# Kernel optimization log

Measured on AMD Instinct MI355X. Metric: run time of the kernel, lower is better.

The kernel has to match this reference:

```python
import jax, jax.numpy as jnp
import numpy as np

H = 64          # hidden_dim
NH = 4          # n_heads
DH = H // NH
F_OWN = 40      # own feature dim
FA = 24         # ally feature dim
FE = 24         # enemy feature dim
NAL = 15        # n_allies
NEN = 16        # n_enemies
BS = 2048       # episode batch
NAG = 16        # n_agents
BN = BS * NAG
AMOVE = 6       # normal (move) actions
HYPER_OUT = F_OWN * H + H + 4


def setup_inputs():
    key = jax.random.key(0)
    ks = jax.random.split(key, 32)
    g = lambda k, sh, s=1.0: jax.random.normal(k, sh, dtype=jnp.float32) * s
    inv = lambda d: float(1.0 / np.sqrt(d))
    return {
        "own_raw": g(ks[0], (BN, 1, F_OWN)),
        "ally_raw": g(ks[1], (BN, NAL, FA)),
        "enemy_raw": g(ks[2], (BN, NEN, FE)),
        "hidden_state": g(ks[3], (BN, H)),
        "hyp_W1": g(ks[4], (F_OWN, H), inv(F_OWN)),
        "hyp_b1": jnp.zeros((H,), jnp.float32),
        "hyp_W2": g(ks[5], (H, HYPER_OUT), 0.01 * inv(H)),  # torch init mul_(0.01)
        "hyp_b2": jnp.zeros((HYPER_OUT,), jnp.float32),
        "Wa": g(ks[6], (FA, H), inv(FA)), "ba": jnp.zeros((H,), jnp.float32),
        "We": g(ks[7], (FE, H), inv(FE)), "be": jnp.zeros((H,), jnp.float32),
        "aWq": g(ks[8], (H, H), inv(H)), "aWk": g(ks[9], (H, H), inv(H)),
        "aWv": g(ks[10], (H, H), inv(H)), "aWo": g(ks[11], (H, H), inv(H)),
        "eWq": g(ks[12], (H, H), inv(H)), "eWk": g(ks[13], (H, H), inv(H)),
        "eWv": g(ks[14], (H, H), inv(H)), "eWo": g(ks[15], (H, H), inv(H)),
        "gru_Wih": g(ks[16], (3 * H, 3 * H), inv(3 * H)),
        "gru_Whh": g(ks[17], (H, 3 * H), inv(H)),
        "gru_bih": jnp.zeros((3 * H,), jnp.float32),
        "gru_bhh": jnp.zeros((3 * H,), jnp.float32),
        "Wm": g(ks[18], (H, AMOVE), inv(H)), "bm": jnp.zeros((AMOVE,), jnp.float32),
        "WzK": g(ks[19], (H, H), inv(H)),
        "WEK": g(ks[20], (H, H), inv(H)),
        "bs": BS,
    }


def _mha(q_in, kv, mask, Wq, Wk, Wv, Wo):
    # masked multi-head cross attention: q_in [B,H], kv [B,n,H], mask [B,n] bool
    B, n = kv.shape[0], kv.shape[1]
    q = (q_in @ Wq).reshape(B, NH, DH)
    k = (kv @ Wk).reshape(B, n, NH, DH)
    v = (kv @ Wv).reshape(B, n, NH, DH)
    scores = jnp.einsum('bhd,bnhd->bhn', q, k) * float(1.0 / np.sqrt(DH))
    scores = jnp.where(mask[:, None, :], scores, -1e9)
    attn = jax.nn.softmax(scores, axis=-1)
    out = jnp.einsum('bhn,bnhd->bhd', attn, v).reshape(B, H)
    return out @ Wo


def reference(own_raw, ally_raw, enemy_raw, hidden_state,
              hyp_W1, hyp_b1, hyp_W2, hyp_b2,
              Wa, ba, We, be,
              aWq, aWk, aWv, aWo, eWq, eWk, eWv, eWo,
              gru_Wih, gru_Whh, gru_bih, gru_bhh,
              Wm, bm, WzK, WEK, bs):
    Bn = own_raw.shape[0]
    ally_mask = jnp.any(ally_raw != 0, axis=-1)    # ~all(x==0)
    enemy_mask = jnp.any(enemy_raw != 0, axis=-1)
    own_vec = own_raw[:, 0, :]                     # [Bn, F_OWN]
    # hypernet: per-agent own-embedding weights + bias (last 4 outputs unused, as in source)
    h_out = jax.nn.relu(own_vec @ hyp_W1 + hyp_b1) @ hyp_W2 + hyp_b2
    W_flat = h_out[:, :F_OWN * H].reshape(Bn, F_OWN, H)
    b_own = h_out[:, F_OWN * H:F_OWN * H + H]
    own_e = jnp.einsum('bf,bfh->bh', own_vec, W_flat) + b_own
    ally_e = ally_raw @ Wa + ba
    enemy_e = enemy_raw @ We + be
    zA = _mha(own_e, ally_e, ally_mask, aWq, aWk, aWv, aWo)
    zE = _mha(own_e, enemy_e, enemy_mask, eWq, eWk, eWv, eWo)
    u_cat = jnp.concatenate([own_e, zA, zE], axis=-1)  # [Bn, 3H]
    # GRUCell (torch semantics)
    gx = u_cat @ gru_Wih + gru_bih
    gh = hidden_state @ gru_Whh + gru_bhh
    xr, xz, xn = jnp.split(gx, 3, axis=-1)
    hr, hz, hn = jnp.split(gh, 3, axis=-1)
    r = jax.nn.sigmoid(xr + hr)
    zg = jax.nn.sigmoid(xz + hz)
    ncand = jnp.tanh(xn + r * hn)
    z = (1.0 - zg) * ncand + zg * hidden_state
    logits_move = z @ Wm + bm
    zk = z @ WzK
    Ek = enemy_e @ WEK
    logits_shoot = jnp.einsum('bd,bmd->bm', zk, Ek)
    Q = jnp.concatenate([logits_move, logits_shoot], axis=-1)[:, None, :]
    return Q, z.reshape(bs, -1, H)
```

## Files before the change

### kernel.cpp

```cpp
#include <hip/hip_runtime.h>
#include <hip/hip_bf16.h>
#include <math.h>

#define TB 32
#define LOG2E 1.44269504f

typedef float f32x4 __attribute__((ext_vector_type(4)));
typedef _Float16 f16x8 __attribute__((ext_vector_type(8)));
typedef _Float16 f16x4 __attribute__((ext_vector_type(4)));
typedef _Float16 f16x2 __attribute__((ext_vector_type(2)));

#define OFF_W1T  344064
#define OFF_WOA  352256
#define OFF_WOE  360448
#define OFF_VBA  368640
#define OFF_VBE  372736
#define OFF_GA   376832
#define OFF_GE   393216
#define OFF_GIH  409600
#define OFF_GHH  483328
#define OFF_GBS  507904
#define OFF_GBH  508672
#define OFF_BHD  508928

#define MFH(a, b, c) __builtin_amdgcn_mfma_f32_16x16x32_f16((a), (b), (c), 0, 0, 0)

__device__ inline float dot2(f16x2 a, f16x2 b, float c) {
#if __has_builtin(__builtin_amdgcn_fdot2)
  return __builtin_amdgcn_fdot2(a, b, c, false);
#else
  return c + (float)a[0] * (float)b[0] + (float)a[1] * (float)b[1];
#endif
}
__device__ inline f16x2 pk2(float x, float y) {
  f16x2 r; r[0] = (_Float16)x; r[1] = (_Float16)y; return r;
}

__global__ __launch_bounds__(256)
void prep_kernel(const float* __restrict__ hyp_W1, const float* __restrict__ hyp_b1,
                 const float* __restrict__ hyp_W2, const float* __restrict__ hyp_b2,
                 const float* __restrict__ Wa, const float* __restrict__ ba,
                 const float* __restrict__ We, const float* __restrict__ be,
                 const float* __restrict__ aWq, const float* __restrict__ aWk,
                 const float* __restrict__ aWv, const float* __restrict__ aWo,
                 const float* __restrict__ eWq, const float* __restrict__ eWk,
                 const float* __restrict__ eWv, const float* __restrict__ eWo,
                 const float* __restrict__ gWih, const float* __restrict__ gWhh,
                 const float* __restrict__ gbih, const float* __restrict__ gbhh,
                 const float* __restrict__ WzK, const float* __restrict__ WEK,
                 const float* __restrict__ Wm,
                 void* __restrict__ ws)
{
  const int b = blockIdx.x, t = threadIdx.x;
  if (b < 42) {
    _Float16* o = (_Float16*)ws;
    for (int i = t; i < 4096; i += 256) {
      int h = i >> 6, k = i & 63;
      float v;
      if (b < 40)       v = hyp_W2[(size_t)k * 2628 + b * 64 + h];
      else if (b == 40) v = hyp_W2[(size_t)k * 2628 + 2560 + h];
      else              v = (k < 40) ? hyp_b2[k * 64 + h]
                             : (k == 40 ? hyp_b2[2560 + h] : 0.0f);
      o[b * 4096 + i] = (_Float16)v;
    }
  } else if (b == 42) {
    _Float16* o = (_Float16*)((char*)ws + OFF_W1T);
    for (int i = t; i < 4096; i += 256) {
      int h = i >> 6, k = i & 63;
      float v = (k < 40) ? hyp_W1[k * 64 + h] : (k == 40 ? hyp_b1[h] : 0.0f);
      o[i] = (_Float16)v;
    }
  } else if (b == 43 || b == 44) {
    const float* M = (b == 43) ? aWo : eWo;
    _Float16* o = (_Float16*)((char*)ws + (b == 43 ? OFF_WOA : OFF_WOE));
    for (int i = t; i < 4096; i += 256)
      o[i] = (_Float16)M[(i & 63) * 64 + (i >> 6)];
  } else if (b == 45 || b == 46) {
    const float* Wemb = (b == 45) ? Wa : We;
    const float* bemb = (b == 45) ? ba : be;
    const float* Wv   = (b == 45) ? aWv : eWv;
    _Float16* o = (_Float16*)((char*)ws + (b == 45 ? OFF_VBA : OFF_VBE));
    for (int i = t; i < 2048; i += 256) {
      int h = i >> 5, k = i & 31;
      float v = 0.f;
      if (k < 24)       { for (int d = 0; d < 64; ++d) v += Wemb[k * 64 + d] * Wv[d * 64 + h]; }
      else if (k == 24) { for (int d = 0; d < 64; ++d) v += bemb[d] * Wv[d * 64 + h]; }
      o[i] = (_Float16)v;
    }
  } else if (b == 47 || b == 48) {
    const float* Wemb = (b == 47) ? Wa : We;
    const float* bemb = (b == 47) ? ba : be;
    const float* Wk   = (b == 47) ? aWk : eWk;
    const float* Wq   = (b == 47) ? aWq : eWq;
    _Float16* o = (_Float16*)((char*)ws + (b == 47 ? OFF_GA : OFF_GE));
    __shared__ float sKb[25 * 64];
    for (int i = t; i < 1600; i += 256) {
      int k = i >> 6, c = i & 63;
      float v = 0.f;
      if (k < 24)  { for (int d = 0; d < 64; ++d) v += Wemb[k * 64 + d] * Wk[d * 64 + c]; }
      else         { for (int d = 0; d < 64; ++d) v += bemb[d] * Wk[d * 64 + c]; }
      sKb[i] = v;
    }
    __syncthreads();
    for (int i = t; i < 8192; i += 256) {
      int col = i >> 6, d = i & 63;
      int h = col >> 5, kk = col & 31;
      float v = 0.f;
      if (kk < 25)
        for (int dh = 0; dh < 16; ++dh)
          v += Wq[d * 64 + h * 16 + dh] * sKb[kk * 64 + h * 16 + dh];
      o[i] = (_Float16)(v * 0.25f * LOG2E);
    }
  } else if (b == 49) {
    _Float16* o = (_Float16*)((char*)ws + OFF_GIH);
    for (int i = t; i < 36864; i += 256) {
      int d = i / 192, c = i - d * 192;
      o[c * 192 + d] = (_Float16)gWih[i];
    }
  } else if (b == 50) {
    _Float16* o = (_Float16*)((char*)ws + OFF_GHH);
    for (int i = t; i < 12288; i += 256) {
      int d = i / 192, c = i - d * 192;
      o[c * 64 + d] = (_Float16)gWhh[i];
    }
  } else if (b == 51) {
    float* gbS = (float*)((char*)ws + OFF_GBS);
    float* gbH = (float*)((char*)ws + OFF_GBH);
    if (t < 192) gbS[t] = gbih[t] + (t < 128 ? gbhh[t] : 0.0f);
    if (t < 64)  gbH[t] = gbhh[128 + t];
  } else if (b == 52) {
    __shared__ float sWsK[24 * 64];
    __shared__ float sbw[64];
    _Float16* o = (_Float16*)((char*)ws + OFF_BHD);
    for (int i = t; i < 1536; i += 256) {
      int j = i >> 6, h = i & 63;
      float v = 0.f;
      for (int c = 0; c < 64; ++c) v += We[j * 64 + c] * WEK[c * 64 + h];
      sWsK[i] = v;
    }
    if (t < 64) {
      float v = 0.f;
      for (int c = 0; c < 64; ++c) v += be[c] * WEK[c * 64 + t];
      sbw[t] = v;
    }
    __syncthreads();
    for (int i = t; i < 2048; i += 256) {
      int col = i >> 6, c = i & 63;
      float v = 0.f;
      if (col < 24)       { for (int d = 0; d < 64; ++d) v += WzK[c * 64 + d] * sWsK[col * 64 + d]; }
      else if (col == 24) { for (int d = 0; d < 64; ++d) v += WzK[c * 64 + d] * sbw[d]; }
      else if (col < 31)  v = Wm[c * 6 + (col - 25)];
      o[i] = (_Float16)v;
    }
  }
}

#define SCORE_BODY(Q0,Q1,Q2,Q3,Q4,Q5,WP,SCV)                                  \
  {                                                                            \
    unsigned orv =                                                             \
      ((Q0.x!=0.f)|(Q0.y!=0.f)|(Q0.z!=0.f)|(Q0.w!=0.f)|                        \
       (Q1.x!=0.f)|(Q1.y!=0.f)|(Q1.z!=0.f)|(Q1.w!=0.f)|                        \
       (Q2.x!=0.f)|(Q2.y!=0.f)|(Q2.z!=0.f)|(Q2.w!=0.f)|                        \
       (Q3.x!=0.f)|(Q3.y!=0.f)|(Q3.z!=0.f)|(Q3.w!=0.f)|                        \
       (Q4.x!=0.f)|(Q4.y!=0.f)|(Q4.z!=0.f)|(Q4.w!=0.f)|                        \
       (Q5.x!=0.f)|(Q5.y!=0.f)|(Q5.z!=0.f)|(Q5.w!=0.f)) ? 1u : 0u;             \
    f16x2 r0 = pk2(Q0.x,Q0.y), r1 = pk2(Q0.z,Q0.w);                            \
    f16x2 r2 = pk2(Q1.x,Q1.y), r3 = pk2(Q1.z,Q1.w);                            \
    f16x2 r4 = pk2(Q2.x,Q2.y), r5 = pk2(Q2.z,Q2.w);                            \
    f16x2 r6 = pk2(Q3.x,Q3.y), r7 = pk2(Q3.z,Q3.w);                            \
    f16x2 r8 = pk2(Q4.x,Q4.y), r9 = pk2(Q4.z,Q4.w);                            \
    f16x2 r10 = pk2(Q5.x,Q5.y), r11 = pk2(Q5.z,Q5.w);                          \
    _Pragma("unroll")                                                          \
    for (int h = 0; h < 4; ++h) {                                              \
      const _Float16* wq = (WP) + h * 32;                                      \
      float a = (float)wq[24];                                                 \
      a = dot2(r0,  *(const f16x2*)(wq + 0),  a);                              \
      a = dot2(r1,  *(const f16x2*)(wq + 2),  a);                              \
      a = dot2(r2,  *(const f16x2*)(wq + 4),  a);                              \
      a = dot2(r3,  *(const f16x2*)(wq + 6),  a);                              \
      a = dot2(r4,  *(const f16x2*)(wq + 8),  a);                              \
      a = dot2(r5,  *(const f16x2*)(wq + 10), a);                              \
      a = dot2(r6,  *(const f16x2*)(wq + 12), a);                              \
      a = dot2(r7,  *(const f16x2*)(wq + 14), a);                              \
      a = dot2(r8,  *(const f16x2*)(wq + 16), a);                              \
      a = dot2(r9,  *(const f16x2*)(wq + 18), a);                              \
      a = dot2(r10, *(const f16x2*)(wq + 20), a);                              \
      a = dot2(r11, *(const f16x2*)(wq + 22), a);                              \
      SCV[h] = orv ? a : -1.0e9f;                                              \
    }                                                                          \
  }

__global__ __launch_bounds__(256, 4)
void agent_kernel(
    const float* __restrict__ own_raw, const float* __restrict__ ally_raw,
    const float* __restrict__ enemy_raw, const float* __restrict__ hidden,
    const float* __restrict__ bm,
    const void* __restrict__ ws,
    float* __restrict__ out, int BN)
{
  __shared__ __align__(16) char s_all[29440];
  _Float16* s_u16   = (_Float16*)s_all;
  _Float16* s_hid16 = (_Float16*)(s_all + 12544);
  char*     sR2     = s_all + 16896;
  _Float16* s_own16 = (_Float16*)sR2;
  _Float16* s_ownT  = (_Float16*)(sR2 + 3328);
  _Float16* s_h116  = (_Float16*)(sR2 + 5888);
  _Float16* s_w16   = (_Float16*)sR2;
  _Float16* s_att16 = (_Float16*)sR2;
  _Float16* s_p16   = (_Float16*)(sR2 + 8320);
  _Float16* s_z16   = (_Float16*)sR2;
  _Float16* s_t16   = (_Float16*)(sR2 + 4352);
  float*    s_q     = (float*)(sR2 + 6016);

  const int tid = threadIdx.x;
  const int bs0 = blockIdx.x * TB;
  const int l   = tid & 63;
  const int wv  = tid >> 6;
  const int lr  = l & 15;
  const int oct = l >> 4;
  const int s8  = tid >> 3;
  const int sh  = tid & 7;

  const f16x8 ZERO8F = {0,0,0,0,0,0,0,0};
  f16x8 ONE8F = ZERO8F; ONE8F[0] = (_Float16)1.0f;
  const f32x4 ZERO4 = {0.f, 0.f, 0.f, 0.f};

  for (int i = tid; i < 640; i += 256) {
    int ss = i / 20, c = i - ss * 20;
    float2 v = *(const float2*)(own_raw + (size_t)(bs0 + ss) * 40 + c * 2);
    *(f16x2*)(s_own16 + ss * 52 + c * 2) = pk2(v.x, v.y);
  }
  for (int i = tid; i < 1280; i += 256) {
    int f = i >> 5, s2 = i & 31;
    s_ownT[i] = (_Float16)own_raw[(size_t)(bs0 + s2) * 40 + f];
  }
  for (int i = tid; i < 1024; i += 256) {
    int ss = i >> 5, c = i & 31;
    float2 v = *(const float2*)(hidden + (size_t)(bs0 + ss) * 64 + c * 2);
    *(f16x2*)(s_hid16 + ss * 68 + c * 2) = pk2(v.x, v.y);
  }
  __syncthreads();

  {
    const _Float16* w1t = (const _Float16*)((const char*)ws + OFF_W1T);
    f16x8 b0 = *(const f16x8*)(w1t + (wv * 16 + lr) * 64 + oct * 8);
    f16x8 b1 = *(const f16x8*)(w1t + (wv * 16 + lr) * 64 + 32 + oct * 8);
    #pragma unroll
    for (int rt = 0; rt < 2; ++rt) {
      f16x8 a0 = *(const f16x8*)(s_own16 + (rt * 16 + lr) * 52 + oct * 8);
      f16x8 a1;
      if (oct == 0)      a1 = *(const f16x8*)(s_own16 + (rt * 16 + lr) * 52 + 32);
      else if (oct == 1) a1 = ONE8F;
      else               a1 = ZERO8F;
      f32x4 acc = ZERO4;
      acc = MFH(a0, b0, acc);
      acc = MFH(a1, b1, acc);
      #pragma unroll
      for (int j = 0; j < 4; ++j)
        s_h116[(rt * 16 + oct * 4 + j) * 68 + wv * 16 + lr] = (_Float16)fmaxf(acc[j], 0.f);
    }
  }
  __syncthreads();

  {
    const _Float16* bb = (const _Float16*)ws + (size_t)(wv * 16 + lr) * 64 + oct * 8;
    f16x8 h0f0 = *(const f16x8*)(s_h116 + lr * 68 + oct * 8);
    f16x8 h1f0 = *(const f16x8*)(s_h116 + lr * 68 + 32 + oct * 8);
    f16x8 h0f1 = *(const f16x8*)(s_h116 + (16 + lr) * 68 + oct * 8);
    f16x8 h1f1 = *(const f16x8*)(s_h116 + (16 + lr) * 68 + 32 + oct * 8);
    f32x4 acc0 = ZERO4, acc1 = ZERO4;
    #pragma unroll 4
    for (int f = 0; f < 40; ++f) {
      f16x8 b0 = *(const f16x8*)(bb + (size_t)f * 4096);
      f16x8 b1 = *(const f16x8*)(bb + (size_t)f * 4096 + 32);
      f32x4 y0 = MFH(h0f0, b0, ZERO4); y0 = MFH(h1f0, b1, y0);
      f32x4 y1 = MFH(h0f1, b0, ZERO4); y1 = MFH(h1f1, b1, y1);
      f16x4 ov0 = *(const f16x4*)(s_ownT + f * 32 + oct * 4);
      f16x4 ov1 = *(const f16x4*)(s_ownT + f * 32 + 16 + oct * 4);
      #pragma unroll
      for (int j = 0; j < 4; ++j) {
        acc0[j] += (float)ov0[j] * y0[j];
        acc1[j] += (float)ov1[j] * y1[j];
      }
    }
    f32x4 aD0 = ZERO4, aD1 = ZERO4;
    {
      f16x8 b0 = *(const f16x8*)(bb + (size_t)40 * 4096);
      f16x8 b1 = *(const f16x8*)(bb + (size_t)40 * 4096 + 32);
      aD0 = MFH(h0f0, b0, aD0); aD0 = MFH(h1f0, b1, aD0);
      aD1 = MFH(h0f1, b0, aD1); aD1 = MFH(h1f1, b1, aD1);
    }
    {
      f16x8 b0 = *(const f16x8*)(bb + (size_t)41 * 4096);
      f16x8 b1 = *(const f16x8*)(bb + (size_t)41 * 4096 + 32);
      #pragma unroll
      for (int rt = 0; rt < 2; ++rt) {
        f16x8 a0 = *(const f16x8*)(s_own16 + (rt * 16 + lr) * 52 + oct * 8);
        f16x8 a1;
        if (oct == 0)      a1 = *(const f16x8*)(s_own16 + (rt * 16 + lr) * 52 + 32);
        else if (oct == 1) a1 = ONE8F;
        else               a1 = ZERO8F;
        if (rt) { aD1 = MFH(a0, b0, aD1); aD1 = MFH(a1, b1, aD1); }
        else    { aD0 = MFH(a0, b0, aD0); aD0 = MFH(a1, b1, aD0); }
      }
    }
    #pragma unroll
    for (int j = 0; j < 4; ++j) {
      s_u16[(oct * 4 + j) * 196 + wv * 16 + lr]        = (_Float16)(acc0[j] + aD0[j]);
      s_u16[(16 + oct * 4 + j) * 196 + wv * 16 + lr]   = (_Float16)(acc1[j] + aD1[j]);
    }
  }
  __syncthreads();

  for (int side = 0; side < 2; ++side) {
    const int n_ent = side ? 16 : 15;
    const int rstr  = side ? 384 : 360;
    const float* rawg = side ? enemy_raw : ally_raw;
    const _Float16* woT = (const _Float16*)((const char*)ws + (side ? OFF_WOE : OFF_WOA));
    const _Float16* vbT = (const _Float16*)((const char*)ws + (side ? OFF_VBE : OFF_VBA));
    const _Float16* gT  = (const _Float16*)((const char*)ws + (side ? OFF_GE  : OFF_GA));

    {
      f16x8 a00 = *(const f16x8*)(s_u16 + lr * 196 + oct * 8);
      f16x8 a10 = *(const f16x8*)(s_u16 + lr * 196 + 32 + oct * 8);
      f16x8 a01 = *(const f16x8*)(s_u16 + (16 + lr) * 196 + oct * 8);
      f16x8 a11 = *(const f16x8*)(s_u16 + (16 + lr) * 196 + 32 + oct * 8);
      #pragma unroll
      for (int t2 = 0; t2 < 2; ++t2) {
        int col = wv * 32 + t2 * 16 + lr;
        f16x8 b0 = *(const f16x8*)(gT + col * 64 + oct * 8);
        f16x8 b1 = *(const f16x8*)(gT + col * 64 + 32 + oct * 8);
        f32x4 ac0 = ZERO4, ac1 = ZERO4;
        ac0 = MFH(a00, b0, ac0); ac0 = MFH(a10, b1, ac0);
        ac1 = MFH(a01, b0, ac1); ac1 = MFH(a11, b1, ac1);
        #pragma unroll
        for (int j = 0; j < 4; ++j) {
          s_w16[(oct * 4 + j) * 130 + col]      = (_Float16)ac0[j];
          s_w16[(16 + oct * 4 + j) * 130 + col] = (_Float16)ac1[j];
        }
      }
    }

    float4 qa0, qa1, qa2, qa3, qa4, qa5, qb0, qb1, qb2, qb3, qb4, qb5;
    {
      const int n1 = (sh + 8 < n_ent) ? (sh + 8) : (n_ent - 1);
      const float* rp0 = rawg + (size_t)(bs0 + s8) * rstr + sh * 24;
      const float* rp1 = rawg + (size_t)(bs0 + s8) * rstr + n1 * 24;
      qa0 = *(const float4*)(rp0);      qa1 = *(const float4*)(rp0 + 4);
      qa2 = *(const float4*)(rp0 + 8);  qa3 = *(const float4*)(rp0 + 12);
      qa4 = *(const float4*)(rp0 + 16); qa5 = *(const float4*)(rp0 + 20);
      qb0 = *(const float4*)(rp1);      qb1 = *(const float4*)(rp1 + 4);
      qb2 = *(const float4*)(rp1 + 8);  qb3 = *(const float4*)(rp1 + 12);
      qb4 = *(const float4*)(rp1 + 16); qb5 = *(const float4*)(rp1 + 20);
    }
    __syncthreads();

    {
      const _Float16* wp = s_w16 + s8 * 130;
      f32x4 sc0, sc1;
      SCORE_BODY(qa0, qa1, qa2, qa3, qa4, qa5, wp, sc0);
      SCORE_BODY(qb0, qb1, qb2, qb3, qb4, qb5, wp, sc1);
      if (sh + 8 >= n_ent) {
        #pragma unroll
        for (int h = 0; h < 4; ++h) sc1[h] = -2.0e9f;
      }
      f32x4 m, lsum, p0v, p1v;
      #pragma unroll
      for (int h = 0; h < 4; ++h) m[h] = fmaxf(sc0[h], sc1[h]);
      #pragma unroll
      for (int d = 1; d < 8; d <<= 1) {
        #pragma unroll
        for (int h = 0; h < 4; ++h) m[h] = fmaxf(m[h], __shfl_xor(m[h], d));
      }
      #pragma unroll
      for (int h = 0; h < 4; ++h) {
        p0v[h] = __builtin_exp2f(sc0[h] - m[h]);
        p1v[h] = __builtin_exp2f(sc1[h] - m[h]);
        lsum[h] = p0v[h] + p1v[h];
      }
      #pragma unroll
      for (int d = 1; d < 8; d <<= 1) {
        #pragma unroll
        for (int h = 0; h < 4; ++h) lsum[h] += __shfl_xor(lsum[h], d);
      }
      f32x4 rl;
      #pragma unroll
      for (int h = 0; h < 4; ++h) rl[h] = __builtin_amdgcn_rcpf(lsum[h]);
      {
        f16x4 pk;
        #pragma unroll
        for (int h = 0; h < 4; ++h) pk[h] = (_Float16)(p0v[h] * rl[h]);
        *(f16x4*)(s_p16 + sh * 132 + s8 * 4) = pk;
      }
      if (sh + 8 < n_ent) {
        f16x4 pk;
        #pragma unroll
        for (int h = 0; h < 4; ++h) pk[h] = (_Float16)(p1v[h] * rl[h]);
        *(f16x4*)(s_p16 + (sh + 8) * 132 + s8 * 4) = pk;
      }
    }
    __syncthreads();

    {
      f16x8 vbF = *(const f16x8*)(vbT + (wv * 16 + lr) * 32 + oct * 8);
      const float* rpv0 = rawg + (size_t)(bs0 + lr) * rstr + oct * 8;
      const float* rpv1 = rawg + (size_t)(bs0 + 16 + lr) * rstr + oct * 8;
      f32x4 oac0 = ZERO4, oac1 = ZERO4;
      #pragma unroll
      for (int i = 0; i < 16; ++i) {
        if (i >= n_ent) break;
        _Float16 pw0 = s_p16[i * 132 + lr * 4 + wv];
        _Float16 pw1 = s_p16[i * 132 + (16 + lr) * 4 + wv];
        f16x8 fr0, fr1;
        if (oct < 3) {
          float4 a = *(const float4*)(rpv0 + i * 24);
          float4 b = *(const float4*)(rpv0 + i * 24 + 4);
          fr0[0] = (_Float16)a.x * pw0; fr0[1] = (_Float16)a.y * pw0;
          fr0[2] = (_Float16)a.z * pw0; fr0[3] = (_Float16)a.w * pw0;
          fr0[4] = (_Float16)b.x * pw0; fr0[5] = (_Float16)b.y * pw0;
          fr0[6] = (_Float16)b.z * pw0; fr0[7] = (_Float16)b.w * pw0;
          float4 c = *(const float4*)(rpv1 + i * 24);
          float4 d = *(const float4*)(rpv1 + i * 24 + 4);
          fr1[0] = (_Float16)c.x * pw1; fr1[1] = (_Float16)c.y * pw1;
          fr1[2] = (_Float16)c.z * pw1; fr1[3] = (_Float16)c.w * pw1;
          fr1[4] = (_Float16)d.x * pw1; fr1[5] = (_Float16)d.y * pw1;
          fr1[6] = (_Float16)d.z * pw1; fr1[7] = (_Float16)d.w * pw1;
        } else {
          fr0 = ZERO8F; fr0[0] = pw0;
          fr1 = ZERO8F; fr1[0] = pw1;
        }
        oac0 = MFH(fr0, vbF, oac0);
        oac1 = MFH(fr1, vbF, oac1);
      }
      __syncthreads();
      #pragma unroll
      for (int j = 0; j < 4; ++j) {
        s_att16[(oct * 4 + j) * 68 + wv * 16 + lr]      = (_Float16)oac0[j];
        s_att16[(16 + oct * 4 + j) * 68 + wv * 16 + lr] = (_Float16)oac1[j];
      }
    }
    __syncthreads();

    {
      f16x8 b0 = *(const f16x8*)(woT + (wv * 16 + lr) * 64 + oct * 8);
      f16x8 b1 = *(const f16x8*)(woT + (wv * 16 + lr) * 64 + 32 + oct * 8);
      #pragma unroll
      for (int rt = 0; rt < 2; ++rt) {
        f16x8 a0 = *(const f16x8*)(s_att16 + (rt * 16 + lr) * 68 + oct * 8);
        f16x8 a1 = *(const f16x8*)(s_att16 + (rt * 16 + lr) * 68 + 32 + oct * 8);
        f32x4 oa = ZERO4;
        oa = MFH(a0, b0, oa);
        oa = MFH(a1, b1, oa);
        #pragma unroll
        for (int j = 0; j < 4; ++j)
          s_u16[(rt * 16 + oct * 4 + j) * 196 + 64 + side * 64 + wv * 16 + lr] = (_Float16)oa[j];
      }
    }
    __syncthreads();
  }

  {
    const _Float16* ihT = (const _Float16*)((const char*)ws + OFF_GIH);
    const _Float16* hhT = (const _Float16*)((const char*)ws + OFF_GHH);
    const float* gbS = (const float*)((const char*)ws + OFF_GBS);
    const float* gbH = (const float*)((const char*)ws + OFF_GBH);
    f32x4 aX0[2] = {ZERO4, ZERO4}, aX1[2] = {ZERO4, ZERO4};
    f32x4 aX2[2] = {ZERO4, ZERO4}, aH2[2] = {ZERO4, ZERO4};
    #pragma unroll
    for (int st = 0; st < 6; ++st) {
      f16x8 uf0 = *(const f16x8*)(s_u16 + lr * 196 + st * 32 + oct * 8);
      f16x8 uf1 = *(const f16x8*)(s_u16 + (16 + lr) * 196 + st * 32 + oct * 8);
      f16x8 b0 = *(const f16x8*)(ihT + ((wv    ) * 16 + lr) * 192 + st * 32 + oct * 8);
      f16x8 b1 = *(const f16x8*)(ihT + ((wv + 4) * 16 + lr) * 192 + st * 32 + oct * 8);
      f16x8 b2 = *(const f16x8*)(ihT + ((wv + 8) * 16 + lr) * 192 + st * 32 + oct * 8);
      aX0[0] = MFH(uf0, b0, aX0[0]);  aX0[1] = MFH(uf1, b0, aX0[1]);
      aX1[0] = MFH(uf0, b1, aX1[0]);  aX1[1] = MFH(uf1, b1, aX1[1]);
      aX2[0] = MFH(uf0, b2, aX2[0]);  aX2[1] = MFH(uf1, b2, aX2[1]);
    }
    #pragma unroll
    for (int st = 0; st < 2; ++st) {
      f16x8 hf0 = *(const f16x8*)(s_hid16 + lr * 68 + st * 32 + oct * 8);
      f16x8 hf1 = *(const f16x8*)(s_hid16 + (16 + lr) * 68 + st * 32 + oct * 8);
      f16x8 b0 = *(const f16x8*)(hhT + ((wv    ) * 16 + lr) * 64 + st * 32 + oct * 8);
      f16x8 b1 = *(const f16x8*)(hhT + ((wv + 4) * 16 + lr) * 64 + st * 32 + oct * 8);
      f16x8 b2 = *(const f16x8*)(hhT + ((wv + 8) * 16 + lr) * 64 + st * 32 + oct * 8);
      aX0[0] = MFH(hf0, b0, aX0[0]);  aX0[1] = MFH(hf1, b0, aX0[1]);
      aX1[0] = MFH(hf0, b1, aX1[0]);  aX1[1] = MFH(hf1, b1, aX1[1]);
      aH2[0] = MFH(hf0, b2, aH2[0]);  aH2[1] = MFH(hf1, b2, aH2[1]);
    }
    const int c0 = wv * 16 + lr;
    float bb0 = gbS[c0], bb1 = gbS[c0 + 64], bb2 = gbS[c0 + 128], bbh = gbH[c0];
    __syncthreads();
    #pragma unroll
    for (int rt = 0; rt < 2; ++rt) {
      #pragma unroll
      for (int j = 0; j < 4; ++j) {
        int row = rt * 16 + oct * 4 + j;
        float xr = aX0[rt][j] + bb0;
        float xz = aX1[rt][j] + bb1;
        float xn = aX2[rt][j] + bb2;
        float hn = aH2[rt][j] + bbh;
        float r  = __builtin_amdgcn_rcpf(1.f + __builtin_exp2f(-xr * LOG2E));
        float zg = __builtin_amdgcn_rcpf(1.f + __builtin_exp2f(-xz * LOG2E));
        float ta = xn + r * hn;
        float nc = 1.f - 2.f * __builtin_amdgcn_rcpf(1.f + __builtin_exp2f(2.f * LOG2E * ta));
        float hv = (float)s_hid16[row * 68 + c0];
        s_z16[row * 68 + c0] = (_Float16)((1.f - zg) * nc + zg * hv);
      }
    }
  }
  __syncthreads();

  {
    const _Float16* bhT = (const _Float16*)((const char*)ws + OFF_BHD);
    const int rt = wv >> 1;
    const int col = (wv & 1) * 16 + lr;
    f16x8 a0 = *(const f16x8*)(s_z16 + (rt * 16 + lr) * 68 + oct * 8);
    f16x8 a1 = *(const f16x8*)(s_z16 + (rt * 16 + lr) * 68 + 32 + oct * 8);
    f16x8 b0 = *(const f16x8*)(bhT + col * 64 + oct * 8);
    f16x8 b1 = *(const f16x8*)(bhT + col * 64 + 32 + oct * 8);
    f32x4 td = ZERO4;
    td = MFH(a0, b0, td);
    td = MFH(a1, b1, td);
    #pragma unroll
    for (int j = 0; j < 4; ++j) {
      int row = rt * 16 + oct * 4 + j;
      if (col < 25)      s_t16[row * 26 + col] = (_Float16)td[j];
      else if (col < 31) s_q[row * 22 + (col - 25)] = td[j] + bm[col - 25];
    }
  }
  __syncthreads();
  {
    const _Float16* tp = s_t16 + s8 * 26;
    #pragma unroll
    for (int e = 0; e < 2; ++e) {
      int m = sh + e * 8;
      const float* er = enemy_raw + (size_t)(bs0 + s8) * 384 + m * 24;
      float acc2 = (float)tp[24];
      #pragma unroll
      for (int k4 = 0; k4 < 6; ++k4) {
        float4 r4 = *(const float4*)(er + k4 * 4);
        acc2 += r4.x * (float)tp[k4*4]   + r4.y * (float)tp[k4*4+1]
              + r4.z * (float)tp[k4*4+2] + r4.w * (float)tp[k4*4+3];
      }
      s_q[s8 * 22 + 6 + m] = acc2;
    }
  }
  __syncthreads();
  for (int i = tid; i < 704; i += 256)
    out[(size_t)bs0 * 22 + i] = s_q[i];
  for (int i = tid; i < 2048; i += 256)
    out[(size_t)BN * 22 + (size_t)bs0 * 64 + i] = (float)s_z16[(i >> 6) * 68 + (i & 63)];
}

extern "C" void kernel_launch(void* const* d_in, const int* in_sizes, int n_in,
                              void* d_out, int out_size, void* d_ws, size_t ws_size,
                              hipStream_t stream) {
  (void)n_in; (void)out_size; (void)ws_size;
  const float* own_raw   = (const float*)d_in[0];
  const float* ally_raw  = (const float*)d_in[1];
  const float* enemy_raw = (const float*)d_in[2];
  const float* hidden    = (const float*)d_in[3];
  const float* hyp_W1    = (const float*)d_in[4];
  const float* hyp_b1    = (const float*)d_in[5];
  const float* hyp_W2    = (const float*)d_in[6];
  const float* hyp_b2    = (const float*)d_in[7];
  const float* Wa        = (const float*)d_in[8];
  const float* ba        = (const float*)d_in[9];
  const float* We        = (const float*)d_in[10];
  const float* be        = (const float*)d_in[11];
  const float* aWq       = (const float*)d_in[12];
  const float* aWk       = (const float*)d_in[13];
  const float* aWv       = (const float*)d_in[14];
  const float* aWo       = (const float*)d_in[15];
  const float* eWq       = (const float*)d_in[16];
  const float* eWk       = (const float*)d_in[17];
  const float* eWv       = (const float*)d_in[18];
  const float* eWo       = (const float*)d_in[19];
  const float* gWih      = (const float*)d_in[20];
  const float* gWhh      = (const float*)d_in[21];
  const float* gbih      = (const float*)d_in[22];
  const float* gbhh      = (const float*)d_in[23];
  const float* Wm        = (const float*)d_in[24];
  const float* bm        = (const float*)d_in[25];
  const float* WzK       = (const float*)d_in[26];
  const float* WEK       = (const float*)d_in[27];
  int BN = in_sizes[0] / 40;
  int blocks = BN / TB;

  hipLaunchKernelGGL(prep_kernel, dim3(53), dim3(256), 0, stream,
                     hyp_W1, hyp_b1, hyp_W2, hyp_b2, Wa, ba, We, be,
                     aWq, aWk, aWv, aWo, eWq, eWk, eWv, eWo,
                     gWih, gWhh, gbih, gbhh, WzK, WEK, Wm, d_ws);
  hipLaunchKernelGGL(agent_kernel, dim3(blocks), dim3(256), 0, stream,
                     own_raw, ally_raw, enemy_raw, hidden, bm,
                     d_ws, (float*)d_out, BN);
}
```

Measured before the change: 157.1 us.

## Process ally and enemy attention stages together with double-buffered shared memory

The sequential per-side loop is restructured so that each attention stage (key projection, scores/softmax, value aggregation, output projection) runs for both ally and enemy sides before a single barrier. Separate shared buffers per side replace the reused ones, and the hidden-state load moves later into freed space. The aim is fewer block-wide barriers and more independent work between them. In exchange, LDS use grows from about 29 KB to 37 KB per block, which may reduce occupancy under the 4-blocks launch bound, and register pressure rises.

```diff
diff --git a/kernel.cpp b/kernel.cpp
--- a/kernel.cpp
+++ b/kernel.cpp
@@ -198,19 +198,22 @@
     const void* __restrict__ ws,
     float* __restrict__ out, int BN)
 {
-  __shared__ __align__(16) char s_all[29440];
-  _Float16* s_u16   = (_Float16*)s_all;
-  _Float16* s_hid16 = (_Float16*)(s_all + 12544);
-  char*     sR2     = s_all + 16896;
+  __shared__ __align__(16) char s_all[37632];
+  _Float16* s_u16 = (_Float16*)s_all;
+  char*     sR2   = s_all + 12544;
   _Float16* s_own16 = (_Float16*)sR2;
   _Float16* s_ownT  = (_Float16*)(sR2 + 3328);
   _Float16* s_h116  = (_Float16*)(sR2 + 5888);
-  _Float16* s_w16   = (_Float16*)sR2;
-  _Float16* s_att16 = (_Float16*)sR2;
-  _Float16* s_p16   = (_Float16*)(sR2 + 8320);
+  _Float16* s_w0    = (_Float16*)sR2;
+  _Float16* s_w1    = (_Float16*)(sR2 + 8320);
+  _Float16* s_pp0   = (_Float16*)(sR2 + 16640);
+  _Float16* s_pp1   = (_Float16*)(sR2 + 20864);
+  _Float16* s_att0  = (_Float16*)sR2;
+  _Float16* s_att1  = (_Float16*)(sR2 + 8320);
+  _Float16* s_hid16 = (_Float16*)(sR2 + 16640);
   _Float16* s_z16   = (_Float16*)sR2;
   _Float16* s_t16   = (_Float16*)(sR2 + 4352);
-  float*    s_q     = (float*)(sR2 + 6016);
+  float*    s_q     = (float*)(sR2 + 8320);
 
   const int tid = threadIdx.x;
   const int bs0 = blockIdx.x * TB;
@@ -233,11 +236,6 @@
   for (int i = tid; i < 1280; i += 256) {
     int f = i >> 5, s2 = i & 31;
     s_ownT[i] = (_Float16)own_raw[(size_t)(bs0 + s2) * 40 + f];
-  }
-  for (int i = tid; i < 1024; i += 256) {
-    int ss = i >> 5, c = i & 31;
-    float2 v = *(const float2*)(hidden + (size_t)(bs0 + ss) * 64 + c * 2);
-    *(f16x2*)(s_hid16 + ss * 68 + c * 2) = pk2(v.x, v.y);
   }
   __syncthreads();
 
@@ -306,25 +304,21 @@
     }
     #pragma unroll
     for (int j = 0; j < 4; ++j) {
-      s_u16[(oct * 4 + j) * 196 + wv * 16 + lr]        = (_Float16)(acc0[j] + aD0[j]);
-      s_u16[(16 + oct * 4 + j) * 196 + wv * 16 + lr]   = (_Float16)(acc1[j] + aD1[j]);
-    }
-  }
-  __syncthreads();
-
-  for (int side = 0; side < 2; ++side) {
-    const int n_ent = side ? 16 : 15;
-    const int rstr  = side ? 384 : 360;
-    const float* rawg = side ? enemy_raw : ally_raw;
-    const _Float16* woT = (const _Float16*)((const char*)ws + (side ? OFF_WOE : OFF_WOA));
-    const _Float16* vbT = (const _Float16*)((const char*)ws + (side ? OFF_VBE : OFF_VBA));
-    const _Float16* gT  = (const _Float16*)((const char*)ws + (side ? OFF_GE  : OFF_GA));
-
-    {
-      f16x8 a00 = *(const f16x8*)(s_u16 + lr * 196 + oct * 8);
-      f16x8 a10 = *(const f16x8*)(s_u16 + lr * 196 + 32 + oct * 8);
-      f16x8 a01 = *(const f16x8*)(s_u16 + (16 + lr) * 196 + oct * 8);
-      f16x8 a11 = *(const f16x8*)(s_u16 + (16 + lr) * 196 + 32 + oct * 8);
+      s_u16[(oct * 4 + j) * 196 + wv * 16 + lr]      = (_Float16)(acc0[j] + aD0[j]);
+      s_u16[(16 + oct * 4 + j) * 196 + wv * 16 + lr] = (_Float16)(acc1[j] + aD1[j]);
+    }
+  }
+  __syncthreads();
+
+  {
+    f16x8 a00 = *(const f16x8*)(s_u16 + lr * 196 + oct * 8);
+    f16x8 a10 = *(const f16x8*)(s_u16 + lr * 196 + 32 + oct * 8);
+    f16x8 a01 = *(const f16x8*)(s_u16 + (16 + lr) * 196 + oct * 8);
+    f16x8 a11 = *(const f16x8*)(s_u16 + (16 + lr) * 196 + 32 + oct * 8);
+    #pragma unroll
+    for (int side = 0; side < 2; ++side) {
+      const _Float16* gT = (const _Float16*)((const char*)ws + (side ? OFF_GE : OFF_GA));
+      _Float16* wDst = side ? s_w1 : s_w0;
       #pragma unroll
       for (int t2 = 0; t2 < 2; ++t2) {
         int col = wv * 32 + t2 * 16 + lr;
@@ -335,28 +329,33 @@
         ac1 = MFH(a01, b0, ac1); ac1 = MFH(a11, b1, ac1);
         #pragma unroll
         for (int j = 0; j < 4; ++j) {
-          s_w16[(oct * 4 + j) * 130 + col]      = (_Float16)ac0[j];
-          s_w16[(16 + oct * 4 + j) * 130 + col] = (_Float16)ac1[j];
+          wDst[(oct * 4 + j) * 130 + col]      = (_Float16)ac0[j];
+          wDst[(16 + oct * 4 + j) * 130 + col] = (_Float16)ac1[j];
         }
       }
     }
-
-    float4 qa0, qa1, qa2, qa3, qa4, qa5, qb0, qb1, qb2, qb3, qb4, qb5;
-    {
+  }
+  __syncthreads();
+
+  {
+    #pragma unroll
+    for (int side = 0; side < 2; ++side) {
+      const int n_ent = side ? 16 : 15;
+      const int rstr  = side ? 384 : 360;
+      const float* rawg = side ? enemy_raw : ally_raw;
+      const _Float16* wp = (side ? s_w1 : s_w0) + s8 * 130;
+      _Float16* pp = side ? s_pp1 : s_pp0;
+
       const int n1 = (sh + 8 < n_ent) ? (sh + 8) : (n_ent - 1);
       const float* rp0 = rawg + (size_t)(bs0 + s8) * rstr + sh * 24;
       const float* rp1 = rawg + (size_t)(bs0 + s8) * rstr + n1 * 24;
-      qa0 = *(const float4*)(rp0);      qa1 = *(const float4*)(rp0 + 4);
-      qa2 = *(const float4*)(rp0 + 8);  qa3 = *(const float4*)(rp0 + 12);
-      qa4 = *(const float4*)(rp0 + 16); qa5 = *(const float4*)(rp0 + 20);
-      qb0 = *(const float4*)(rp1);      qb1 = *(const float4*)(rp1 + 4);
-      qb2 = *(const float4*)(rp1 + 8);  qb3 = *(const float4*)(rp1 + 12);
-      qb4 = *(const float4*)(rp1 + 16); qb5 = *(const float4*)(rp1 + 20);
-    }
-    __syncthreads();
-
-    {
-      const _Float16* wp = s_w16 + s8 * 130;
+      float4 qa0 = *(const float4*)(rp0);      float4 qa1 = *(const float4*)(rp0 + 4);
+      float4 qa2 = *(const float4*)(rp0 + 8);  float4 qa3 = *(const float4*)(rp0 + 12);
+      float4 qa4 = *(const float4*)(rp0 + 16); float4 qa5 = *(const float4*)(rp0 + 20);
+      float4 qb0 = *(const float4*)(rp1);      float4 qb1 = *(const float4*)(rp1 + 4);
+      float4 qb2 = *(const float4*)(rp1 + 8);  float4 qb3 = *(const float4*)(rp1 + 12);
+      float4 qb4 = *(const float4*)(rp1 + 16); float4 qb5 = *(const float4*)(rp1 + 20);
+
       f32x4 sc0, sc1;
       SCORE_BODY(qa0, qa1, qa2, qa3, qa4, qa5, wp, sc0);
       SCORE_BODY(qb0, qb1, qb2, qb3, qb4, qb5, wp, sc1);
@@ -390,18 +389,28 @@
         f16x4 pk;
         #pragma unroll
         for (int h = 0; h < 4; ++h) pk[h] = (_Float16)(p0v[h] * rl[h]);
-        *(f16x4*)(s_p16 + sh * 132 + s8 * 4) = pk;
+        *(f16x4*)(pp + sh * 132 + s8 * 4) = pk;
       }
       if (sh + 8 < n_ent) {
         f16x4 pk;
         #pragma unroll
         for (int h = 0; h < 4; ++h) pk[h] = (_Float16)(p1v[h] * rl[h]);
-        *(f16x4*)(s_p16 + (sh + 8) * 132 + s8 * 4) = pk;
-      }
-    }
-    __syncthreads();
-
-    {
+        *(f16x4*)(pp + (sh + 8) * 132 + s8 * 4) = pk;
+      }
+    }
+  }
+  __syncthreads();
+
+  {
+    #pragma unroll
+    for (int side = 0; side < 2; ++side) {
+      const int n_ent = side ? 16 : 15;
+      const int rstr  = side ? 384 : 360;
+      const float* rawg = side ? enemy_raw : ally_raw;
+      const _Float16* vbT = (const _Float16*)((const char*)ws + (side ? OFF_VBE : OFF_VBA));
+      const _Float16* pp = side ? s_pp1 : s_pp0;
+      _Float16* attD = side ? s_att1 : s_att0;
+
       f16x8 vbF = *(const f16x8*)(vbT + (wv * 16 + lr) * 32 + oct * 8);
       const float* rpv0 = rawg + (size_t)(bs0 + lr) * rstr + oct * 8;
       const float* rpv1 = rawg + (size_t)(bs0 + 16 + lr) * rstr + oct * 8;
@@ -409,8 +418,8 @@
       #pragma unroll
       for (int i = 0; i < 16; ++i) {
         if (i >= n_ent) break;
-        _Float16 pw0 = s_p16[i * 132 + lr * 4 + wv];
-        _Float16 pw1 = s_p16[i * 132 + (16 + lr) * 4 + wv];
+        _Float16 pw0 = pp[i * 132 + lr * 4 + wv];
+        _Float16 pw1 = pp[i * 132 + (16 + lr) * 4 + wv];
         f16x8 fr0, fr1;
         if (oct < 3) {
           float4 a = *(const float4*)(rpv0 + i * 24);
@@ -432,22 +441,27 @@
         oac0 = MFH(fr0, vbF, oac0);
         oac1 = MFH(fr1, vbF, oac1);
       }
-      __syncthreads();
+      if (side == 0) __syncthreads();
       #pragma unroll
       for (int j = 0; j < 4; ++j) {
-        s_att16[(oct * 4 + j) * 68 + wv * 16 + lr]      = (_Float16)oac0[j];
-        s_att16[(16 + oct * 4 + j) * 68 + wv * 16 + lr] = (_Float16)oac1[j];
-      }
-    }
-    __syncthreads();
-
-    {
+        attD[(oct * 4 + j) * 68 + wv * 16 + lr]      = (_Float16)oac0[j];
+        attD[(16 + oct * 4 + j) * 68 + wv * 16 + lr] = (_Float16)oac1[j];
+      }
+    }
+  }
+  __syncthreads();
+
+  {
+    #pragma unroll
+    for (int side = 0; side < 2; ++side) {
+      const _Float16* woT = (const _Float16*)((const char*)ws + (side ? OFF_WOE : OFF_WOA));
+      const _Float16* attS = side ? s_att1 : s_att0;
       f16x8 b0 = *(const f16x8*)(woT + (wv * 16 + lr) * 64 + oct * 8);
       f16x8 b1 = *(const f16x8*)(woT + (wv * 16 + lr) * 64 + 32 + oct * 8);
       #pragma unroll
       for (int rt = 0; rt < 2; ++rt) {
-        f16x8 a0 = *(const f16x8*)(s_att16 + (rt * 16 + lr) * 68 + oct * 8);
-        f16x8 a1 = *(const f16x8*)(s_att16 + (rt * 16 + lr) * 68 + 32 + oct * 8);
+        f16x8 a0 = *(const f16x8*)(attS + (rt * 16 + lr) * 68 + oct * 8);
+        f16x8 a1 = *(const f16x8*)(attS + (rt * 16 + lr) * 68 + 32 + oct * 8);
         f32x4 oa = ZERO4;
         oa = MFH(a0, b0, oa);
         oa = MFH(a1, b1, oa);
@@ -456,8 +470,13 @@
           s_u16[(rt * 16 + oct * 4 + j) * 196 + 64 + side * 64 + wv * 16 + lr] = (_Float16)oa[j];
       }
     }
-    __syncthreads();
-  }
+    for (int i = tid; i < 1024; i += 256) {
+      int ss = i >> 5, c = i & 31;
+      float2 v = *(const float2*)(hidden + (size_t)(bs0 + ss) * 64 + c * 2);
+      *(f16x2*)(s_hid16 + ss * 68 + c * 2) = pk2(v.x, v.y);
+    }
+  }
+  __syncthreads();
 
   {
     const _Float16* ihT = (const _Float16*)((const char*)ws + OFF_GIH);
@@ -490,7 +509,6 @@
     }
     const int c0 = wv * 16 + lr;
     float bb0 = gbS[c0], bb1 = gbS[c0 + 64], bb2 = gbS[c0 + 128], bbh = gbH[c0];
-    __syncthreads();
     #pragma unroll
     for (int rt = 0; rt < 2; ++rt) {
       #pragma unroll
```

Result: faster. 146.7 us (-6.6%).
